# Kernel tuning notes

Measured on AMD Instinct MI355X. Metric: run time of the kernel, lower is better.

The kernel has to match this reference:

```python
import jax, jax.numpy as jnp
import numpy as np
from itertools import product

N_CODONS = 2
ORDER = 2
N_STATES = 25          # calc_number_of_states() with nCodons=2
ALPHA6 = 6             # alphabet_size + 2
OFFSET = 8 + 3 * N_CODONS       # 14, first insert state
TERM1 = OFFSET + 3 * (N_CODONS + 1)  # 23, terminal_1 state

CODE = {'A': [0], 'C': [1], 'G': [2], 'T': [3], 'N': [0, 1, 2, 3], 'X': [5]}


def _state_entries(state, emissions, x_must_preceed):
    ems = ['N'] * (ORDER - len(emissions) + 1) + list(emissions)[-(ORDER + 1):]
    allowed = [[state]]
    for i, e in enumerate(ems):
        allowed.append(CODE[e] + ([4] if i < ORDER - x_must_preceed else []))
    out = []
    for x in product(*allowed):
        found, ok = False, True
        for i in range(1, ORDER + 1):
            if found and x[i] == 4:
                ok = False
                break
            if x[i] != 4:
                found = True
        if ok:
            out.append(x)
    return out


def _emission_index_spec():
    entries, k = [], 0
    def add(state, ems, xp, trainable=True):
        nonlocal k
        ids = _state_entries(state, ems, xp)
        for t, x in enumerate(ids):
            entries.append((x, k + t if trainable else -1))
        if trainable:
            k += len(ids)
    add(0, 'N', 0); add(1, 'A', 0); add(2, 'AT', 0); add(3, 'ATG', 0, False)
    add(4, 'ATGN', 0); add(5, 'ATGNN', 0)
    for s in range(6, 6 + N_CODONS * 3 - 2):
        add(s, 'N', 0)
    add(4 + 3 * N_CODONS, 'T', ORDER)
    add(5 + 3 * N_CODONS, 'TA', ORDER); add(5 + 3 * N_CODONS, 'TG', ORDER)
    add(6 + 3 * N_CODONS, 'TAA', ORDER, False)
    add(6 + 3 * N_CODONS, 'TAG', ORDER, False)
    add(6 + 3 * N_CODONS, 'TGA', ORDER, False)
    add(7 + 3 * N_CODONS, 'N', ORDER)
    for s in range(8 + 3 * N_CODONS, 8 + 3 * N_CODONS + 3 * (N_CODONS + 1)):
        add(s, 'N', 0)
    for i in range(1, ORDER + 1):
        add(TERM1, 'X' * i, ORDER)
    add(TERM1 + 1, 'X' * (ORDER + 1), ORDER, False)
    idx = np.array([e[0] for e in entries], dtype=np.int32)
    widx = np.array([e[1] for e in entries], dtype=np.int32)
    return idx, widx

EM_IDX, EM_WIDX = _emission_index_spec()


def build_A(w):
    # sparse transition structure -> row-softmax over nonzeros -> dense [25,25]
    idx, vals = [], []
    def add(i, j, v):
        idx.append((i, j)); vals.append(v)
    n, k = N_CODONS, 0
    add(0, 0, 1 - w[k]); add(0, 1, w[k]); k += 1
    add(1, 2, 1.0); add(2, 3, 1.0)
    for i in range(n):
        add(3 + 3 * i, 4 + 3 * i, w[k + i])
    k += n
    for i in range(n):
        add(4 + 3 * i, 5 + 3 * i, 1.0)
    for i in range(n):
        add(5 + 3 * i, 6 + 3 * i, 1.0)
    for i in range(n + 1):
        add(3 + 3 * i, OFFSET + 3 * i, w[k + i])
    k += n + 1
    add(3 + 3 * n, 4 + 3 * n, 1 - w[k - 1])
    for i in range(n + 1):
        add(OFFSET + 3 * i, OFFSET + 1 + 3 * i, 1.0)
    for i in range(n + 1):
        add(OFFSET + 1 + 3 * i, OFFSET + 2 + 3 * i, 1.0)
    for i in range(n + 1):
        add(OFFSET + 2 + 3 * i, 4 + 3 * i, w[k + i])
    for i in range(n + 1):
        add(OFFSET + 2 + 3 * i, OFFSET + 3 * i, 1 - w[k + i])
    k += n + 1
    i_del = [3 + 3 * i for i in range(n) for _ in range(n - i)]
    j_del = [4 + 3 * j for i in range(1, n + 1) for j in range(i, n + 1)]
    for i, j in zip(i_del, j_del):
        add(i, j, 1 - w[k] * w[k] ** ((j - i) // 3))
    k += 1
    add(4 + 3 * n, 5 + 3 * n, 1.0); add(5 + 3 * n, 6 + 3 * n, 1.0)
    add(6 + 3 * n, 7 + 3 * n, 1.0)
    add(7 + 3 * n, 7 + 3 * n, 1.0); add(7 + 3 * n, TERM1, 1.0)
    add(TERM1, TERM1, 1.0); add(TERM1, TERM1 + 1, 1.0)
    add(TERM1 + 1, TERM1 + 1, 1.0)
    rows = np.array([i for i, _ in idx]); cols = np.array([j for _, j in idx])
    logits = jnp.stack([jnp.asarray(v, jnp.float32) for v in vals])
    M = jnp.full((N_STATES, N_STATES), -jnp.inf, jnp.float32).at[rows, cols].set(logits)
    A = jax.nn.softmax(M, axis=-1)
    return jnp.where(jnp.isfinite(M), A, 0.0)


def build_B(w):
    # sparse emission values (trainable weights or fixed 1), per-state softmax over nonzeros
    vals = jnp.where(EM_WIDX >= 0, w[np.clip(EM_WIDX, 0, None)], 1.0)
    rows = EM_IDX[:, 0]
    flat = EM_IDX[:, 1] * 36 + EM_IDX[:, 2] * 6 + EM_IDX[:, 3]
    M = jnp.full((N_STATES, ALPHA6 ** 3), -jnp.inf, jnp.float32).at[rows, flat].set(vals)
    B = jax.nn.softmax(M, axis=-1)
    return jnp.where(jnp.isfinite(M), B, 0.0)  # [25, 216]


def build_I(w):
    n_init = 3 + 3 * N_CODONS  # states 0..8 get initial mass
    p = jax.nn.softmax(w[:n_init])
    return jnp.zeros((N_STATES,), jnp.float32).at[:n_init].set(p)


def _forward(transition_kernel, emission_kernel, init_kernel, tokens):
    A = build_A(transition_kernel)
    Bf = build_B(emission_kernel)
    I = build_I(init_kernel)
    Bt, T = tokens.shape
    pad = jnp.full((Bt, ORDER), 4, tokens.dtype)  # '4' = no preceding emission
    tp = jnp.concatenate([pad, tokens], axis=1)
    flat = tp[:, :-2] * 36 + tp[:, 1:-1] * 6 + tp[:, 2:]  # [Bt, T]
    E = jnp.moveaxis(Bf.T[flat], 1, 0)  # [T, Bt, 25]
    alpha = I[None, :] * E[0]
    s = alpha.sum(-1, keepdims=True)
    alpha = alpha / s
    ll = jnp.log(s[..., 0])
    def step(carry, e):
        a, ll = carry
        a = (a @ A) * e
        s = a.sum(-1, keepdims=True)
        return (a / s, ll + jnp.log(s[..., 0])), None
    (alpha, ll), _ = jax.lax.scan(step, (alpha, ll), E[1:])
    return ll  # [Bt] per-sequence log-likelihood


def setup_inputs() -> dict:
    key = jax.random.key(0)
    k1, k2, k3, k4 = jax.random.split(key, 4)
    return {
        'transition_kernel': jax.random.normal(k1, (10,), jnp.float32) * 0.05,
        'emission_kernel': jax.random.normal(k2, (5400,), jnp.float32) * 0.05,
        'init_kernel': jax.random.normal(k3, (25,), jnp.float32) * 0.05,
        'tokens': jax.random.randint(k4, (512, 2048), 0, 4, jnp.int32),
    }


def reference(transition_kernel, emission_kernel, init_kernel, tokens):
    return _forward(transition_kernel, emission_kernel, init_kernel, tokens)
```

## Files before the change

kernel.cpp:

```cpp
#include <hip/hip_runtime.h>
#include <hip/hip_bf16.h>
#include <math.h>


#define NSTATES 25
#define NLIVE   23
#define NFLAT   216
#define TLEN    2048
#define NSEQ    512
#define CHUNKS  16
#define CLEN    128

#define WS_AW 0
#define WS_I  32
#define WS_BT 64

struct WMap { short m[NSTATES * NFLAT]; };

constexpr WMap make_wmap() {
  WMap w{};
  for (int i = 0; i < NSTATES * NFLAT; i++) w.m[i] = -2;
  const unsigned char ST[29] = {0,1,2,3,4,5,6,7,8,9,10,11,11,12,12,12,13,
                                14,15,16,17,18,19,20,21,22,23,23,24};
  const unsigned char M1[29] = {0x1F,0x1F,0x1F,0x11,0x18,0x14,0x1F,0x1F,0x1F,
                                0x1F,0x0F,0x0F,0x0F,0x08,0x08,0x08,0x0F,
                                0x1F,0x1F,0x1F,0x1F,0x1F,0x1F,0x1F,0x1F,0x1F,
                                0x0F,0x0F,0x20};
  const unsigned char M2[29] = {0x1F,0x1F,0x11,0x18,0x14,0x1F,0x1F,0x1F,0x1F,
                                0x1F,0x0F,0x08,0x08,0x01,0x01,0x04,0x0F,
                                0x1F,0x1F,0x1F,0x1F,0x1F,0x1F,0x1F,0x1F,0x1F,
                                0x0F,0x20,0x20};
  const unsigned char M3[29] = {0x0F,0x01,0x08,0x04,0x0F,0x0F,0x0F,0x0F,0x0F,
                                0x0F,0x08,0x01,0x04,0x01,0x04,0x01,0x0F,
                                0x0F,0x0F,0x0F,0x0F,0x0F,0x0F,0x0F,0x0F,0x0F,
                                0x20,0x20,0x20};
  const unsigned char TR[29] = {1,1,1,0,1,1,1,1,1,1,1,1,1,0,0,0,1,
                                1,1,1,1,1,1,1,1,1,1,1,0};
  int k = 0;
  for (int s = 0; s < 29; s++) {
    for (int c1 = 0; c1 < 6; c1++) {
      if (!((M1[s] >> c1) & 1)) continue;
      for (int c2 = 0; c2 < 6; c2++) {
        if (!((M2[s] >> c2) & 1)) continue;
        if (c1 != 4 && c2 == 4) continue;
        for (int c3 = 0; c3 < 6; c3++) {
          if (!((M3[s] >> c3) & 1)) continue;
          w.m[ST[s] * NFLAT + c1 * 36 + c2 * 6 + c3] =
              TR[s] ? (short)(k++) : (short)-1;
        }
      }
    }
  }
  return w;
}
__device__ __constant__ WMap WMAP = make_wmap();

__device__ __forceinline__ unsigned short f2bf(float x) {
  unsigned int u = __float_as_uint(x);
  u += 0x7fffu + ((u >> 16) & 1u);
  return (unsigned short)(u >> 16);
}
__device__ __forceinline__ float bf2f(unsigned short b) {
  return __uint_as_float(((unsigned int)b) << 16);
}

__global__ __launch_bounds__(64)
void setup_kernel(const float* __restrict__ wT, const float* __restrict__ wE,
                  const float* __restrict__ wI, float* __restrict__ ws) {
  const int st = blockIdx.x;
  const int lane = threadIdx.x;

  if (st < NSTATES) {
    float e[4];
    float part = 0.0f;
    int cnt = 0;
    for (int c = lane; c < NFLAT; c += 64, cnt++) {
      short m = WMAP.m[st * NFLAT + c];
      float v = 0.0f;
      if (m == -1) v = expf(1.0f);
      else if (m >= 0) v = expf(wE[m]);
      e[cnt] = v;
      part += v;
    }
    #pragma unroll
    for (int m = 1; m < 64; m <<= 1) part += __shfl_xor(part, m, 64);
    float inv = 1.0f / part;
    cnt = 0;
    for (int c = lane; c < NFLAT; c += 64, cnt++)
      ws[WS_BT + c * 32 + st] = e[cnt] * inv;
  } else {
    if (lane == 0) {
      const float w0 = wT[0], w1 = wT[1], w2 = wT[2], w3 = wT[3], w4 = wT[4];
      const float w5 = wT[5], w6 = wT[6], w7 = wT[7], w8 = wT[8], w9 = wT[9];
      { float e0 = expf(1.0f - w0), e1 = expf(w0), is = 1.0f / (e0 + e1);
        ws[WS_AW + 0] = e0 * is; ws[WS_AW + 1] = e1 * is; }
      { float e4 = expf(w1), e14 = expf(w3);
        float e7 = expf(1.0f - w9 * w9), e10 = expf(1.0f - w9 * w9 * w9);
        float is = 1.0f / (e4 + e14 + e7 + e10);
        ws[WS_AW + 2] = e4 * is;  ws[WS_AW + 3] = e14 * is;
        ws[WS_AW + 4] = e7 * is;  ws[WS_AW + 5] = e10 * is; }
      { float e7 = expf(w2), e17 = expf(w4), e10 = expf(1.0f - w9 * w9);
        float is = 1.0f / (e7 + e17 + e10);
        ws[WS_AW + 6] = e7 * is; ws[WS_AW + 7] = e17 * is; ws[WS_AW + 8] = e10 * is; }
      { float e20 = expf(w5), e10 = expf(1.0f - w5), is = 1.0f / (e20 + e10);
        ws[WS_AW + 9] = e20 * is; ws[WS_AW + 10] = e10 * is; }
      ws[WS_AW + 11] = 0.5f; ws[WS_AW + 12] = 0.5f;
      { float e4 = expf(w6), e14 = expf(1.0f - w6), is = 1.0f / (e4 + e14);
        ws[WS_AW + 13] = e4 * is; ws[WS_AW + 14] = e14 * is; }
      { float e7 = expf(w7), e17 = expf(1.0f - w7), is = 1.0f / (e7 + e17);
        ws[WS_AW + 15] = e7 * is; ws[WS_AW + 16] = e17 * is; }
      { float e10 = expf(w8), e20 = expf(1.0f - w8), is = 1.0f / (e10 + e20);
        ws[WS_AW + 17] = e10 * is; ws[WS_AW + 18] = e20 * is; }
      ws[WS_AW + 19] = 0.5f; ws[WS_AW + 20] = 0.5f;
    } else if (lane == 32) {
      float e[9], s = 0.0f;
      for (int i = 0; i < 9; i++) { e[i] = expf(wI[i]); s += e[i]; }
      float inv = 1.0f / s;
      for (int i = 0; i < 9; i++) ws[WS_I + i] = e[i] * inv;
      for (int i = 9; i < 32; i++) ws[WS_I + i] = 0.0f;
    }
  }
}

__device__ __forceinline__ void hmm_step(float (&a)[NLIVE], const float (&w)[21],
                                         const float* __restrict__ bt, int flat) {
  const float* er = bt + (flat << 5);
  float4 e0 = *(const float4*)(er + 0);
  float4 e1 = *(const float4*)(er + 4);
  float4 e2 = *(const float4*)(er + 8);
  float4 e3 = *(const float4*)(er + 12);
  float4 e4 = *(const float4*)(er + 16);
  float4 e5 = *(const float4*)(er + 20);

  float n0  = a[0]*w[0];
  float n1  = a[0]*w[1];
  float n4  = a[3]*w[2]  + a[16]*w[13];
  float n7  = a[3]*w[4]  + a[6]*w[6]  + a[19]*w[15];
  float n10 = a[3]*w[5]  + a[6]*w[8]  + a[9]*w[10] + a[22]*w[17];
  float n13 = a[12]      + a[13]*w[11];
  float n14 = a[3]*w[3]  + a[16]*w[14];
  float n17 = a[6]*w[7]  + a[19]*w[16];
  float n20 = a[9]*w[9]  + a[22]*w[18];
  float o2 = a[1],  o3 = a[2],  o5 = a[4],  o6 = a[5];
  float o8 = a[7],  o9 = a[8],  o11 = a[10], o12 = a[11];
  float o15 = a[14], o16 = a[15], o18 = a[17], o19 = a[18];
  float o21 = a[20], o22 = a[21];

  a[0] = n0 * e0.x;  a[1] = n1 * e0.y;  a[2] = o2 * e0.z;  a[3] = o3 * e0.w;
  a[4] = n4 * e1.x;  a[5] = o5 * e1.y;  a[6] = o6 * e1.z;  a[7] = n7 * e1.w;
  a[8] = o8 * e2.x;  a[9] = o9 * e2.y;  a[10] = n10 * e2.z; a[11] = o11 * e2.w;
  a[12] = o12 * e3.x; a[13] = n13 * e3.y; a[14] = n14 * e3.z; a[15] = o15 * e3.w;
  a[16] = o16 * e4.x; a[17] = n17 * e4.y; a[18] = o18 * e4.z; a[19] = o19 * e4.w;
  a[20] = n20 * e5.x; a[21] = o21 * e5.y; a[22] = o22 * e5.z;
}

__device__ __forceinline__ void renorm(float (&a)[NLIVE], float& L) {
  float s = (((a[0]+a[1])+(a[2]+a[3])) + ((a[4]+a[5])+(a[6]+a[7])))
          + (((a[8]+a[9])+(a[10]+a[11])) + ((a[12]+a[13])+(a[14]+a[15])))
          + (((a[16]+a[17])+(a[18]+a[19])) + ((a[20]+a[21])+a[22]));
  if (s > 0.0f) {
    L += __logf(s);
    float r = __fdividef(1.0f, s);
    #pragma unroll
    for (int j = 0; j < NLIVE; j++) a[j] *= r;
  } else {
    L = -3.0e38f;
  }
}

__global__ __launch_bounds__(512)
void rows_kernel(const float* __restrict__ ws, const int* __restrict__ tokens,
                 float* __restrict__ out) {
  __shared__ float sBt[NFLAT * 32];
  __shared__ unsigned short sT[CHUNKS * NLIVE * 24];
  __shared__ float sL[CHUNKS * NLIVE];

  for (int i = threadIdx.x; i < NFLAT * 32; i += 512) sBt[i] = ws[WS_BT + i];
  __syncthreads();

  const int seq   = blockIdx.x;
  const int chunk = threadIdx.x >> 5;
  const int row   = threadIdx.x & 31;
  const int* trow = tokens + (size_t)seq * TLEN;
  const int t0    = chunk * CLEN;

  float w[21];
  #pragma unroll
  for (int i = 0; i < 21; i++) w[i] = ws[WS_AW + i];

  float a[NLIVE];
  #pragma unroll
  for (int j = 0; j < NLIVE; j++) a[j] = 0.0f;
  if (row < NLIVE) a[row] = 1.0f;
  float L = 0.0f;

  int p1, p2;
  int4 q0 = *(const int4*)(trow + t0);
  int4 q1 = *(const int4*)(trow + t0 + 4);

  int b = 0;
  if (chunk == 0) {
    p1 = 4; p2 = q0.x;
    int tb[8] = {q0.x, q0.y, q0.z, q0.w, q1.x, q1.y, q1.z, q1.w};
    q0 = *(const int4*)(trow + 8);
    q1 = *(const int4*)(trow + 12);
    #pragma unroll
    for (int u = 1; u < 8; u++) {
      int nt = tb[u];
      hmm_step(a, w, sBt, p1 * 36 + p2 * 6 + nt);
      p1 = p2; p2 = nt;
    }
    renorm(a, L);
    b = 1;
  } else {
    int2 pp = *(const int2*)(trow + t0 - 2);
    p1 = pp.x; p2 = pp.y;
  }

  for (; b < CLEN / 8; b++) {
    int tb[8] = {q0.x, q0.y, q0.z, q0.w, q1.x, q1.y, q1.z, q1.w};
    if (b < CLEN / 8 - 1) {
      q0 = *(const int4*)(trow + t0 + (b + 1) * 8);
      q1 = *(const int4*)(trow + t0 + (b + 1) * 8 + 4);
    }
    #pragma unroll
    for (int u = 0; u < 8; u++) {
      int nt = tb[u];
      hmm_step(a, w, sBt, p1 * 36 + p2 * 6 + nt);
      p1 = p2; p2 = nt;
    }
    renorm(a, L);
  }

  if (row < NLIVE) {
    const int base = (chunk * NLIVE + row) * 24;
    #pragma unroll
    for (int k = 0; k < 11; k++) {
      ushort2 p; p.x = f2bf(a[2 * k]); p.y = f2bf(a[2 * k + 1]);
      *(ushort2*)&sT[base + 2 * k] = p;
    }
    { ushort2 p; p.x = f2bf(a[22]); p.y = 0; *(ushort2*)&sT[base + 22] = p; }
    sL[chunk * NLIVE + row] = L;
  }
  __syncthreads();

  if (threadIdx.x < 64) {
    const int lane = threadIdx.x;
    const bool act = (lane < NLIVE);
    const int jc   = act ? lane : 0;

    const int tok0 = trow[0];
    const int flat0 = 168 + tok0;

    float v = act ? ws[WS_I + lane] * sBt[flat0 * 32 + lane] : 0.0f;
    float s = v;
    #pragma unroll
    for (int m = 1; m < 32; m <<= 1) s += __shfl_xor(s, m, 32);
    float ll = __logf(s);
    v = act ? v * __fdividef(1.0f, s) : 0.0f;

    for (int c = 0; c < CHUNKS; c++) {
      float Lj  = act ? sL[c * NLIVE + lane] : -3.0e38f;
      float key = (act && v > 0.0f) ? Lj : -3.0e38f;
      float mx = key;
      #pragma unroll
      for (int m = 1; m < 32; m <<= 1) mx = fmaxf(mx, __shfl_xor(mx, m, 32));
      float wgt = (act && v > 0.0f) ? v * __expf(Lj - mx) : 0.0f;

      float nv = 0.0f;
      #pragma unroll
      for (int r = 0; r < NLIVE; r++) {
        float wr = __shfl(wgt, r, 64);
        nv += wr * bf2f(sT[(c * NLIVE + r) * 24 + jc]);
      }
      float nva = act ? nv : 0.0f;
      float s2 = nva;
      #pragma unroll
      for (int m = 1; m < 32; m <<= 1) s2 += __shfl_xor(s2, m, 32);
      ll += mx + __logf(s2);
      v = act ? nv * __fdividef(1.0f, s2) : 0.0f;
    }

    if (lane == 0) out[seq] = ll;
  }
}

extern "C" void kernel_launch(void* const* d_in, const int* in_sizes, int n_in,
                              void* d_out, int out_size, void* d_ws, size_t ws_size,
                              hipStream_t stream) {
  const float* wT = (const float*)d_in[0];
  const float* wE = (const float*)d_in[1];
  const float* wI = (const float*)d_in[2];
  const int* tokens = (const int*)d_in[3];
  float* out = (float*)d_out;
  float* ws = (float*)d_ws;

  setup_kernel<<<26, 64, 0, stream>>>(wT, wE, wI, ws);
  rows_kernel<<<NSEQ, 512, 0, stream>>>(ws, tokens, out);
}
```

Measured before the change: 148.4 us.

## Double chunk count, pack emission table to 100 rows, use 1024-thread blocks

```diff
diff --git a/kernel.cpp b/kernel.cpp
--- a/kernel.cpp
+++ b/kernel.cpp
@@ -6,10 +6,11 @@
 #define NSTATES 25
 #define NLIVE   23
 #define NFLAT   216
+#define NPACK   100
 #define TLEN    2048
 #define NSEQ    512
-#define CHUNKS  16
-#define CLEN    128
+#define CHUNKS  32
+#define CLEN    64
 
 #define WS_AW 0
 #define WS_I  32
@@ -71,23 +72,25 @@
   const int lane = threadIdx.x;
 
   if (st < NSTATES) {
-    float e[4];
     float part = 0.0f;
-    int cnt = 0;
-    for (int c = lane; c < NFLAT; c += 64, cnt++) {
+    for (int c = lane; c < NFLAT; c += 64) {
       short m = WMAP.m[st * NFLAT + c];
+      if (m == -1) part += expf(1.0f);
+      else if (m >= 0) part += expf(wE[m]);
+    }
+    #pragma unroll
+    for (int m = 1; m < 64; m <<= 1) part += __shfl_xor(part, m, 64);
+    float inv = 1.0f / part;
+    for (int i = lane; i < NPACK; i += 64) {
+      int c12 = i >> 2, nt = i & 3;
+      int p1 = c12 / 5, p2 = c12 - 5 * p1;
+      int flat = p1 * 36 + p2 * 6 + nt;
+      short m = WMAP.m[st * NFLAT + flat];
       float v = 0.0f;
       if (m == -1) v = expf(1.0f);
       else if (m >= 0) v = expf(wE[m]);
-      e[cnt] = v;
-      part += v;
-    }
-    #pragma unroll
-    for (int m = 1; m < 64; m <<= 1) part += __shfl_xor(part, m, 64);
-    float inv = 1.0f / part;
-    cnt = 0;
-    for (int c = lane; c < NFLAT; c += 64, cnt++)
-      ws[WS_BT + c * 32 + st] = e[cnt] * inv;
+      ws[WS_BT + i * 32 + st] = v * inv;
+    }
   } else {
     if (lane == 0) {
       const float w0 = wT[0], w1 = wT[1], w2 = wT[2], w3 = wT[3], w4 = wT[4];
@@ -123,8 +126,8 @@
 }
 
 __device__ __forceinline__ void hmm_step(float (&a)[NLIVE], const float (&w)[21],
-                                         const float* __restrict__ bt, int flat) {
-  const float* er = bt + (flat << 5);
+                                         const float* __restrict__ bt, int idx) {
+  const float* er = bt + (idx << 5);
   float4 e0 = *(const float4*)(er + 0);
   float4 e1 = *(const float4*)(er + 4);
   float4 e2 = *(const float4*)(er + 8);
@@ -168,14 +171,17 @@
   }
 }
 
-__global__ __launch_bounds__(512)
+#define STEP(nt_) { int nt = (nt_); hmm_step(a, w, sBt, (c12 << 2) + nt); \
+                    c12 = p2 * 5 + nt; p2 = nt; }
+
+__global__ __launch_bounds__(1024)
 void rows_kernel(const float* __restrict__ ws, const int* __restrict__ tokens,
                  float* __restrict__ out) {
-  __shared__ float sBt[NFLAT * 32];
+  __shared__ float sBt[NPACK * 32];
   __shared__ unsigned short sT[CHUNKS * NLIVE * 24];
   __shared__ float sL[CHUNKS * NLIVE];
 
-  for (int i = threadIdx.x; i < NFLAT * 32; i += 512) sBt[i] = ws[WS_BT + i];
+  for (int i = threadIdx.x; i < NPACK * 32; i += 1024) sBt[i] = ws[WS_BT + i];
   __syncthreads();
 
   const int seq   = blockIdx.x;
@@ -186,7 +192,9 @@
 
   float w[21];
   #pragma unroll
-  for (int i = 0; i < 21; i++) w[i] = ws[WS_AW + i];
+  for (int i = 0; i < 21; i++)
+    w[i] = __uint_as_float(
+        (unsigned)__builtin_amdgcn_readfirstlane(__float_as_uint(ws[WS_AW + i])));
 
   float a[NLIVE];
   #pragma unroll
@@ -194,41 +202,26 @@
   if (row < NLIVE) a[row] = 1.0f;
   float L = 0.0f;
 
-  int p1, p2;
-  int4 q0 = *(const int4*)(trow + t0);
-  int4 q1 = *(const int4*)(trow + t0 + 4);
-
+  int c12, p2;
   int b = 0;
   if (chunk == 0) {
-    p1 = 4; p2 = q0.x;
-    int tb[8] = {q0.x, q0.y, q0.z, q0.w, q1.x, q1.y, q1.z, q1.w};
-    q0 = *(const int4*)(trow + 8);
-    q1 = *(const int4*)(trow + 12);
-    #pragma unroll
-    for (int u = 1; u < 8; u++) {
-      int nt = tb[u];
-      hmm_step(a, w, sBt, p1 * 36 + p2 * 6 + nt);
-      p1 = p2; p2 = nt;
-    }
+    int4 q0 = *(const int4*)(trow);
+    int4 q1 = *(const int4*)(trow + 4);
+    c12 = 20 + q0.x; p2 = q0.x;
+    STEP(q0.y); STEP(q0.z); STEP(q0.w);
+    STEP(q1.x); STEP(q1.y); STEP(q1.z); STEP(q1.w);
     renorm(a, L);
     b = 1;
   } else {
     int2 pp = *(const int2*)(trow + t0 - 2);
-    p1 = pp.x; p2 = pp.y;
+    c12 = pp.x * 5 + pp.y; p2 = pp.y;
   }
 
   for (; b < CLEN / 8; b++) {
-    int tb[8] = {q0.x, q0.y, q0.z, q0.w, q1.x, q1.y, q1.z, q1.w};
-    if (b < CLEN / 8 - 1) {
-      q0 = *(const int4*)(trow + t0 + (b + 1) * 8);
-      q1 = *(const int4*)(trow + t0 + (b + 1) * 8 + 4);
-    }
-    #pragma unroll
-    for (int u = 0; u < 8; u++) {
-      int nt = tb[u];
-      hmm_step(a, w, sBt, p1 * 36 + p2 * 6 + nt);
-      p1 = p2; p2 = nt;
-    }
+    int4 q0 = *(const int4*)(trow + t0 + b * 8);
+    int4 q1 = *(const int4*)(trow + t0 + b * 8 + 4);
+    STEP(q0.x); STEP(q0.y); STEP(q0.z); STEP(q0.w);
+    STEP(q1.x); STEP(q1.y); STEP(q1.z); STEP(q1.w);
     renorm(a, L);
   }
 
@@ -250,9 +243,9 @@
     const int jc   = act ? lane : 0;
 
     const int tok0 = trow[0];
-    const int flat0 = 168 + tok0;
-
-    float v = act ? ws[WS_I + lane] * sBt[flat0 * 32 + lane] : 0.0f;
+    const int idx0 = 96 + tok0;
+
+    float v = act ? ws[WS_I + lane] * sBt[idx0 * 32 + lane] : 0.0f;
     float s = v;
     #pragma unroll
     for (int m = 1; m < 32; m <<= 1) s += __shfl_xor(s, m, 32);
@@ -296,5 +289,5 @@
   float* ws = (float*)d_ws;
 
   setup_kernel<<<26, 64, 0, stream>>>(wT, wE, wI, ws);
-  rows_kernel<<<NSEQ, 512, 0, stream>>>(ws, tokens, out);
-}
+  rows_kernel<<<NSEQ, 1024, 0, stream>>>(ws, tokens, out);
+}
```

Result: slower. 174.5 us (+17.5%).
